# Kernel tuning notes

Hardware: AMD Instinct MI355X
Metric: run time of the kernel (lower is better)

## Reference

```python
import jax, jax.numpy as jnp
import numpy as np

B, S, D = 4, 1024, 1024
H = 16           # heads
HD = D // H      # head dim
E = 8            # experts
TOPK = 2
F = 4 * D        # expert ffn hidden


def setup_inputs() -> dict:
    key = jax.random.key(0)
    ks = jax.random.split(key, 8)
    w = lambda k, shp: jax.random.normal(k, shp, dtype=jnp.float32) * 0.02
    return {
        "x": jax.random.normal(ks[0], (B, S, D), dtype=jnp.float32),
        "ln1_g": jnp.ones((D,), jnp.float32), "ln1_b": jnp.zeros((D,), jnp.float32),
        "Wqkv": w(ks[1], (D, 3 * D)),
        "Wo": w(ks[2], (D, D)),
        "ln2_g": jnp.ones((D,), jnp.float32), "ln2_b": jnp.zeros((D,), jnp.float32),
        "Wg": w(ks[3], (D, E)),
        "W1": w(ks[4], (E, D, F)),
        "W2": w(ks[5], (E, F, D)),
    }


def _layernorm(x, g, b, eps=1e-5):
    mu = jnp.mean(x, axis=-1, keepdims=True)
    var = jnp.var(x, axis=-1, keepdims=True)
    return (x - mu) * jax.lax.rsqrt(var + eps) * g + b


def _attn(h, Wqkv, Wo):
    qkv = h @ Wqkv                                   # [B,S,3D]
    q, k, v = jnp.split(qkv, 3, axis=-1)
    q = q.reshape(B, S, H, HD)
    k = k.reshape(B, S, H, HD)
    v = v.reshape(B, S, H, HD)
    scores = jnp.einsum("bqhd,bkhd->bhqk", q, k) / np.sqrt(HD)
    causal = jnp.tril(jnp.ones((S, S), bool))
    scores = jnp.where(causal, scores, jnp.finfo(scores.dtype).min)
    p = jax.nn.softmax(scores, axis=-1)
    o = jnp.einsum("bhqk,bkhd->bqhd", p, v).reshape(B, S, D)
    return o @ Wo


def _moe(h, Wg, W1, W2):
    # h: [N, D] tokens; top-k softmax gating, dense all-expert reference
    logits = h @ Wg                                   # [N, E]
    top_vals, top_idx = jax.lax.top_k(logits, TOPK)   # [N, k]
    wts = jax.nn.softmax(top_vals, axis=-1)           # gate weights over top-k
    gates = jnp.sum(jax.nn.one_hot(top_idx, E) * wts[..., None], axis=1)  # [N, E]
    act = jax.nn.gelu(jnp.einsum("nd,edf->enf", h, W1))  # [E, N, F]
    eo = jnp.einsum("enf,efd->end", act, W2)             # [E, N, D]
    return jnp.einsum("ne,end->nd", gates, eo)           # combine


def reference(x, ln1_g, ln1_b, Wqkv, Wo, ln2_g, ln2_b, Wg, W1, W2):
    h = _layernorm(x, ln1_g, ln1_b)
    x_resid = x + _attn(h, Wqkv, Wo)
    moe_in = _layernorm(x_resid, ln2_g, ln2_b).reshape(B * S, D)
    y = _moe(moe_in, Wg, W1, W2).reshape(B, S, D)
    return x_resid + y
```

## Files before the change

kernel.cpp:

```cpp
#include <hip/hip_runtime.h>

typedef unsigned short u16;
typedef _Float16 f16x8 __attribute__((ext_vector_type(8)));
typedef __bf16   bf16x8 __attribute__((ext_vector_type(8)));
typedef float    f32x4 __attribute__((ext_vector_type(4)));

struct __align__(8) U16x4 { u16 v[4]; };

#define MAXT 72

__device__ __forceinline__ u16 f2b(float f) {
  unsigned u = __builtin_bit_cast(unsigned, f);
  return (u16)((u + 0x7FFFu + ((u >> 16) & 1u)) >> 16);
}
__device__ __forceinline__ u16 f2h(float f) { return __builtin_bit_cast(u16, (_Float16)f); }
__device__ __forceinline__ u16 f2h_lo(float f) {
  _Float16 h = (_Float16)f;
  return __builtin_bit_cast(u16, (_Float16)(f - (float)h));
}
__device__ __forceinline__ void llds16(const void* g, void* l) {
  __builtin_amdgcn_global_load_lds((const __attribute__((address_space(1))) unsigned int*)g,
                                   (__attribute__((address_space(3))) unsigned int*)l, 16, 0, 0);
}
__device__ __forceinline__ f32x4 mmf(f16x8 a, f16x8 b, f32x4 c) {
  return __builtin_amdgcn_mfma_f32_16x16x32_f16(a, b, c, 0, 0, 0);
}
__device__ __forceinline__ f32x4 mmb(bf16x8 a, bf16x8 b, f32x4 c) {
  return __builtin_amdgcn_mfma_f32_16x16x32_bf16(a, b, c, 0, 0, 0);
}

template<int OUT>
__global__ __launch_bounds__(256) void transpose_kernel(const float* __restrict__ src,
                                                        u16* __restrict__ d0, u16* __restrict__ d1,
                                                        int R, int C) {
  __shared__ float t[32][33];
  long zo = (long)blockIdx.z * R * C;
  int r0 = blockIdx.y << 5, c0 = blockIdx.x << 5;
  int tid = threadIdx.x;
  {
    int r = tid >> 3, c = (tid & 7) << 2;
    float4 v = *(const float4*)(src + zo + (long)(r0 + r) * C + c0 + c);
    t[r][c] = v.x; t[r][c + 1] = v.y; t[r][c + 2] = v.z; t[r][c + 3] = v.w;
  }
  __syncthreads();
  int c = tid >> 3, rg = (tid & 7) << 2;
  long o = zo + (long)(c0 + c) * R + r0 + rg;
  U16x4 a, b2;
#pragma unroll
  for (int i = 0; i < 4; i++) {
    float f = t[rg + i][c];
    if (OUT == 0) { a.v[i] = f2h(f); b2.v[i] = f2h_lo(f); }
    else a.v[i] = f2b(f);
  }
  *(U16x4*)(d0 + o) = a;
  if (OUT == 0) *(U16x4*)(d1 + o) = b2;
}

__global__ __launch_bounds__(256) void wg_transpose(const float* __restrict__ Wg,
                                                    float* __restrict__ WgT) {
  int idx = blockIdx.x * 256 + threadIdx.x;
  int d = idx >> 3, e = idx & 7;
  WgT[e * 1024 + d] = Wg[idx];
}

__global__ __launch_bounds__(256) void ln_kernel(const float* __restrict__ x, const float* __restrict__ g,
                                                 const float* __restrict__ bt,
                                                 u16* __restrict__ d0, u16* __restrict__ d1) {
  long row = blockIdx.x;
  int tid = threadIdx.x;
  const float4 v = *(const float4*)(x + (row << 10) + (tid << 2));
  float s = v.x + v.y + v.z + v.w;
  float q = v.x * v.x + v.y * v.y + v.z * v.z + v.w * v.w;
#pragma unroll
  for (int m = 1; m < 64; m <<= 1) { s += __shfl_xor(s, m); q += __shfl_xor(q, m); }
  __shared__ float rs[4], rq[4];
  if ((tid & 63) == 0) { rs[tid >> 6] = s; rq[tid >> 6] = q; }
  __syncthreads();
  s = rs[0] + rs[1] + rs[2] + rs[3];
  q = rq[0] + rq[1] + rq[2] + rq[3];
  float mu = s * (1.f / 1024.f);
  float inv = 1.f / sqrtf(q * (1.f / 1024.f) - mu * mu + 1e-5f);
  float4 gg = *(const float4*)(g + (tid << 2));
  float4 bb = *(const float4*)(bt + (tid << 2));
  float o0 = (v.x - mu) * inv * gg.x + bb.x;
  float o1 = (v.y - mu) * inv * gg.y + bb.y;
  float o2 = (v.z - mu) * inv * gg.z + bb.z;
  float o3 = (v.w - mu) * inv * gg.w + bb.w;
  long o = (row << 10) + (tid << 2);
  U16x4 a, b2;
  a.v[0] = f2h(o0); a.v[1] = f2h(o1); a.v[2] = f2h(o2); a.v[3] = f2h(o3);
  b2.v[0] = f2h_lo(o0); b2.v[1] = f2h_lo(o1); b2.v[2] = f2h_lo(o2); b2.v[3] = f2h_lo(o3);
  *(U16x4*)(d0 + o) = a; *(U16x4*)(d1 + o) = b2;
}

template<int MODE>
__global__ __launch_bounds__(512, 1) void gemm_kernel(
    const u16* __restrict__ Ah, const u16* __restrict__ Al,
    const u16* __restrict__ Bh, const u16* __restrict__ Bl,
    int K, int ldc, int Nexp,
    const int* __restrict__ lists, const int* __restrict__ tile_e,
    const int* __restrict__ tile_b, const int* __restrict__ tile_c,
    float* __restrict__ outf, u16* __restrict__ outb,
    const float* __restrict__ resid, const float* __restrict__ slotw) {
  constexpr bool SPLIT = (MODE < 2);
  constexpr int NP = SPLIT ? 4 : 2;
  constexpr int TN = (MODE == 1) ? 64 : 128;
  constexpr int NF = TN >> 6;
  constexpr int NB = TN >> 6;
  __shared__ u16 lds[NP][8192];
  const int tid = threadIdx.x, w = tid >> 6, l = tid & 63;
  int n0;
  int grbase = 0, rowsv = 128;
  long m0 = 0;
  if (MODE >= 2) {
    int lin = blockIdx.x;
    int c = lin & 7, k = lin >> 3;
    int ty = c * 9 + (k % 9);
    int tx = k / 9;
    n0 = tx * TN;
    int e = tile_e[ty];
    if (e < 0) return;
    grbase = tile_b[ty];
    rowsv = tile_c[ty];
    Bh += (long)e * Nexp * K;
  } else {
    n0 = blockIdx.x * TN;
    m0 = (long)blockIdx.y << 7;
  }

  const u16 *as0[2], *as1[2], *bs0[2], *bs1[2];
  int dstA[2], dstB[2];
#pragma unroll
  for (int i = 0; i < 2; i++) {
    int chunk = i * 512 + tid;
    int row = chunk >> 3, c16 = chunk & 7;
    int scol = (c16 << 4) ^ ((row & 7) << 4);
    dstA[i] = chunk << 4;
    long ar;
    if (MODE == 2) {
      int vlu = lists[(row < rowsv) ? (grbase + row) : grbase];
      ar = (long)(vlu >> 1);
    } else if (MODE == 3) {
      ar = grbase + ((row < rowsv) ? row : 0);
    } else {
      ar = m0 + row;
    }
    long ao = ar * (long)K + (scol >> 1);
    as0[i] = Ah + ao;
    if (SPLIT) as1[i] = Al + ao;
  }
#pragma unroll
  for (int i = 0; i < NB; i++) {
    int chunk = i * 512 + tid;
    int row = chunk >> 3, c16 = chunk & 7;
    int scol = (c16 << 4) ^ ((row & 7) << 4);
    dstB[i] = chunk << 4;
    long bo = (long)(n0 + row) * K + (scol >> 1);
    bs0[i] = Bh + bo;
    if (SPLIT) bs1[i] = Bl + bo;
  }

  f32x4 acc[4][NF];
#pragma unroll
  for (int i = 0; i < 4; i++)
#pragma unroll
    for (int j = 0; j < NF; j++) acc[i][j] = (f32x4){0.f, 0.f, 0.f, 0.f};

  const int wr = (w >> 2) << 6;
  const int wc = (w & 3) * (TN / 4);
  const int nkt = K >> 6;
  for (int kt = 0; kt < nkt; ++kt) {
    if (kt) __syncthreads();
#pragma unroll
    for (int i = 0; i < 2; i++) {
      llds16(as0[i] + (kt << 6), (char*)(&lds[0][0]) + dstA[i]);
      if (SPLIT) llds16(as1[i] + (kt << 6), (char*)(&lds[NP - 2][0]) + dstA[i]);
    }
#pragma unroll
    for (int i = 0; i < NB; i++) {
      llds16(bs0[i] + (kt << 6), (char*)(&lds[1][0]) + dstB[i]);
      if (SPLIT) llds16(bs1[i] + (kt << 6), (char*)(&lds[NP - 1][0]) + dstB[i]);
    }
    __syncthreads();
#pragma unroll
    for (int kc = 0; kc < 2; kc++) {
      const int kby = (kc << 6) + ((l >> 4) << 4);
      int aoff[4], boff[NF];
#pragma unroll
      for (int mf = 0; mf < 4; mf++) { int row = wr + (mf << 4) + (l & 15); aoff[mf] = (row << 7) + (kby ^ ((row & 7) << 4)); }
#pragma unroll
      for (int nf = 0; nf < NF; nf++) { int row = wc + (nf << 4) + (l & 15); boff[nf] = (row << 7) + (kby ^ ((row & 7) << 4)); }
      if (SPLIT) {
        f16x8 a0[4], a1[4], b0[NF], b1[NF];
#pragma unroll
        for (int mf = 0; mf < 4; mf++) {
          a0[mf] = *(const f16x8*)((const char*)(&lds[0][0]) + aoff[mf]);
          a1[mf] = *(const f16x8*)((const char*)(&lds[NP - 2][0]) + aoff[mf]);
        }
#pragma unroll
        for (int nf = 0; nf < NF; nf++) {
          b0[nf] = *(const f16x8*)((const char*)(&lds[1][0]) + boff[nf]);
          b1[nf] = *(const f16x8*)((const char*)(&lds[NP - 1][0]) + boff[nf]);
        }
#pragma unroll
        for (int mf = 0; mf < 4; mf++)
#pragma unroll
          for (int nf = 0; nf < NF; nf++) {
            acc[mf][nf] = mmf(a0[mf], b0[nf], acc[mf][nf]);
            acc[mf][nf] = mmf(a0[mf], b1[nf], acc[mf][nf]);
            acc[mf][nf] = mmf(a1[mf], b0[nf], acc[mf][nf]);
          }
      } else {
        bf16x8 a0[4], b0[NF];
#pragma unroll
        for (int mf = 0; mf < 4; mf++) a0[mf] = *(const bf16x8*)((const char*)(&lds[0][0]) + aoff[mf]);
#pragma unroll
        for (int nf = 0; nf < NF; nf++) b0[nf] = *(const bf16x8*)((const char*)(&lds[1][0]) + boff[nf]);
#pragma unroll
        for (int mf = 0; mf < 4; mf++)
#pragma unroll
          for (int nf = 0; nf < NF; nf++) acc[mf][nf] = mmb(a0[mf], b0[nf], acc[mf][nf]);
      }
    }
  }

#pragma unroll
  for (int mf = 0; mf < 4; mf++) {
#pragma unroll
    for (int r = 0; r < 4; r++) {
      const int lrow = wr + (mf << 4) + ((l >> 4) << 2) + r;
      if (MODE >= 2 && lrow >= rowsv) continue;
      float gw = 0.f; long orow = 0;
      if (MODE == 3) { int gr = grbase + lrow; orow = (long)lists[gr] * ldc; gw = slotw[gr]; }
#pragma unroll
      for (int nf = 0; nf < NF; nf++) {
        const int col = n0 + wc + (nf << 4) + (l & 15);
        float v = acc[mf][nf][r];
        if (MODE == 0) {
          outf[(m0 + lrow) * (long)ldc + col] = v;
        } else if (MODE == 1) {
          long ix = (m0 + lrow) * (long)ldc + col;
          outf[ix] = v + resid[ix];
        } else if (MODE == 2) {
          float t = v * (1.59576912f + 0.07135539f * v * v);
          float u = v * __builtin_amdgcn_rcpf(1.f + __expf(-t));
          outb[(long)(grbase + lrow) * ldc + col] = f2b(u);
        } else {
          outf[orow + col] = v * gw;
        }
      }
    }
  }
}

__global__ __launch_bounds__(256) void kv_prep(const float* __restrict__ qkv,
                                               u16* __restrict__ Kh, u16* __restrict__ Kl,
                                               u16* __restrict__ Vth, u16* __restrict__ Vtl) {
  __shared__ float t[64][65];
  const int tid = threadIdx.x;
  const int kb = blockIdx.x, h = blockIdx.y, b = blockIdx.z;
  const long bb = ((long)b) << 10;
  const int hoff = h << 6;
  const long head = ((long)(b * 16 + h)) << 16;
  {
    int rr = tid >> 4, c = (tid & 15) << 2;
#pragma unroll
    for (int p = 0; p < 4; p++) {
      int r = rr + p * 16;
      const float* base = qkv + (bb + kb * 64 + r) * 3072 + hoff + c;
      float4 u = *(const float4*)(base + 1024);
      U16x4 a, lo;
      a.v[0] = f2h(u.x); a.v[1] = f2h(u.y); a.v[2] = f2h(u.z); a.v[3] = f2h(u.w);
      lo.v[0] = f2h_lo(u.x); lo.v[1] = f2h_lo(u.y); lo.v[2] = f2h_lo(u.z); lo.v[3] = f2h_lo(u.w);
      long o = head + (long)(kb * 64 + r) * 64 + c;
      *(U16x4*)(Kh + o) = a; *(U16x4*)(Kl + o) = lo;
      float4 v = *(const float4*)(base + 2048);
      t[r][c] = v.x; t[r][c + 1] = v.y; t[r][c + 2] = v.z; t[r][c + 3] = v.w;
    }
  }
  __syncthreads();
  {
    int hd = tid >> 2, k4 = (tid & 3) << 4;
#pragma unroll
    for (int q = 0; q < 4; q++) {
      U16x4 a, lo;
#pragma unroll
      for (int j = 0; j < 4; j++) {
        float f = t[k4 + q * 4 + j][hd];
        a.v[j] = f2h(f); lo.v[j] = f2h_lo(f);
      }
      long o = head + (long)hd * 1024 + kb * 64 + k4 + q * 4;
      *(U16x4*)(Vth + o) = a; *(U16x4*)(Vtl + o) = lo;
    }
  }
}

__global__ __launch_bounds__(256, 1) void attn_kernel(const float* __restrict__ qkv,
                                                      const u16* __restrict__ Kh, const u16* __restrict__ Kl,
                                                      const u16* __restrict__ Vth, const u16* __restrict__ Vtl,
                                                      u16* __restrict__ oh, u16* __restrict__ ol) {
  __shared__ u16 kh[4096], kl[4096];
  __shared__ u16 vh[4096], vl[4096];
  __shared__ u16 ph[4][1024], pl[4][1024];
  const int tid = threadIdx.x, w = tid >> 6, l = tid & 63;
  const int qbi = blockIdx.x, hh_ = blockIdx.y, b = blockIdx.z;
  const long bb = ((long)b) << 10;
  const int hoff = hh_ << 6;
  const long head = ((long)(b * 16 + hh_)) << 16;

  const u16 *ks0[2], *ks1[2], *vs0[2], *vs1[2];
  int db[2];
#pragma unroll
  for (int i = 0; i < 2; i++) {
    int chunk = i * 256 + tid;
    int row = chunk >> 3, c16 = chunk & 7;
    int sc = ((c16 << 4) ^ ((row & 7) << 4)) >> 1;
    db[i] = chunk << 4;
    ks0[i] = Kh + head + row * 64 + sc;
    ks1[i] = Kl + head + row * 64 + sc;
    vs0[i] = Vth + head + (long)row * 1024 + sc;
    vs1[i] = Vtl + head + (long)row * 1024 + sc;
  }

  for (int pass = 0; pass < 2; ++pass) {
    const int qb = (pass ? qbi : (15 - qbi)) << 6;
    f16x8 q0[2], q1[2];
    {
      const long qrow = bb + qb + (w << 4) + (l & 15);
      const float* qp = qkv + qrow * 3072 + hoff + ((l >> 4) << 3);
#pragma unroll
      for (int kc = 0; kc < 2; kc++) {
        float4 u0 = *(const float4*)(qp + (kc << 5));
        float4 u1 = *(const float4*)(qp + (kc << 5) + 4);
        float vv[8] = {u0.x, u0.y, u0.z, u0.w, u1.x, u1.y, u1.z, u1.w};
#pragma unroll
        for (int j = 0; j < 8; j++) {
          _Float16 hi = (_Float16)vv[j];
          q0[kc][j] = hi;
          q1[kc][j] = (_Float16)(vv[j] - (float)hi);
        }
      }
    }

    f32x4 o[4];
#pragma unroll
    for (int nf = 0; nf < 4; nf++) o[nf] = (f32x4){0.f, 0.f, 0.f, 0.f};
    float mr[4] = {-1e30f, -1e30f, -1e30f, -1e30f};
    float lr[4] = {0.f, 0.f, 0.f, 0.f};
    const int ktm = qb >> 6;

    for (int kt = 0; kt <= ktm; ++kt) {
      __syncthreads();
#pragma unroll
      for (int i = 0; i < 2; i++) {
        llds16(ks0[i] + (kt << 12), (char*)kh + db[i]);
        llds16(ks1[i] + (kt << 12), (char*)kl + db[i]);
        llds16(vs0[i] + (kt << 6), (char*)vh + db[i]);
        llds16(vs1[i] + (kt << 6), (char*)vl + db[i]);
      }
      __syncthreads();

      f32x4 s[4];
#pragma unroll
      for (int nf = 0; nf < 4; nf++) s[nf] = (f32x4){0.f, 0.f, 0.f, 0.f};
#pragma unroll
      for (int kc = 0; kc < 2; kc++) {
        const int kby = (kc << 6) + ((l >> 4) << 4);
#pragma unroll
        for (int nf = 0; nf < 4; nf++) {
          int row = (nf << 4) + (l & 15);
          int off = (row << 7) + (kby ^ ((row & 7) << 4));
          f16x8 k0 = *(const f16x8*)((const char*)kh + off);
          f16x8 k1 = *(const f16x8*)((const char*)kl + off);
          s[nf] = mmf(q0[kc], k0, s[nf]);
          s[nf] = mmf(q0[kc], k1, s[nf]);
          s[nf] = mmf(q1[kc], k0, s[nf]);
        }
      }
      const bool lastt = (kt == ktm);
#pragma unroll
      for (int nf = 0; nf < 4; nf++)
#pragma unroll
        for (int r = 0; r < 4; r++) {
          float sc = s[nf][r] * 0.125f;
          if (lastt) {
            int keyg = (kt << 6) + (nf << 4) + (l & 15);
            int qg = qb + (w << 4) + ((l >> 4) << 2) + r;
            if (keyg > qg) sc = -1e30f;
          }
          s[nf][r] = sc;
        }
      float alpha[4];
#pragma unroll
      for (int r = 0; r < 4; r++) {
        float mx = fmaxf(fmaxf(s[0][r], s[1][r]), fmaxf(s[2][r], s[3][r]));
        mx = fmaxf(mx, __shfl_xor(mx, 1));
        mx = fmaxf(mx, __shfl_xor(mx, 2));
        mx = fmaxf(mx, __shfl_xor(mx, 4));
        mx = fmaxf(mx, __shfl_xor(mx, 8));
        float mn = fmaxf(mr[r], mx);
        float su = 0.f;
#pragma unroll
        for (int nf = 0; nf < 4; nf++) { float pv = __expf(s[nf][r] - mn); s[nf][r] = pv; su += pv; }
        su += __shfl_xor(su, 1); su += __shfl_xor(su, 2);
        su += __shfl_xor(su, 4); su += __shfl_xor(su, 8);
        alpha[r] = __expf(mr[r] - mn);
        lr[r] = lr[r] * alpha[r] + su;
        mr[r] = mn;
      }
#pragma unroll
      for (int nf = 0; nf < 4; nf++)
#pragma unroll
        for (int r = 0; r < 4; r++) o[nf][r] *= alpha[r];
#pragma unroll
      for (int nf = 0; nf < 4; nf++)
#pragma unroll
        for (int r = 0; r < 4; r++) {
          int m = ((l >> 4) << 2) + r, k = (nf << 4) + (l & 15);
          int off = (m << 7) + ((k << 1) ^ ((m & 7) << 4));
          float pv = s[nf][r];
          _Float16 hi = (_Float16)pv;
          *(u16*)((char*)&ph[w][0] + off) = __builtin_bit_cast(u16, hi);
          *(u16*)((char*)&pl[w][0] + off) = __builtin_bit_cast(u16, (_Float16)(pv - (float)hi));
        }
#pragma unroll
      for (int kc = 0; kc < 2; kc++) {
        const int kby = (kc << 6) + ((l >> 4) << 4);
        const int mm = l & 15;
        int poff = (mm << 7) + (kby ^ ((mm & 7) << 4));
        f16x8 p0 = *(const f16x8*)((const char*)&ph[w][0] + poff);
        f16x8 p1 = *(const f16x8*)((const char*)&pl[w][0] + poff);
#pragma unroll
        for (int nf = 0; nf < 4; nf++) {
          int row = (nf << 4) + (l & 15);
          int off = (row << 7) + (kby ^ ((row & 7) << 4));
          f16x8 v0 = *(const f16x8*)((const char*)vh + off);
          f16x8 v1 = *(const f16x8*)((const char*)vl + off);
          o[nf] = mmf(p0, v0, o[nf]);
          o[nf] = mmf(p0, v1, o[nf]);
          o[nf] = mmf(p1, v0, o[nf]);
        }
      }
    }
#pragma unroll
    for (int nf = 0; nf < 4; nf++)
#pragma unroll
      for (int r = 0; r < 4; r++) {
        int lrow = (w << 4) + ((l >> 4) << 2) + r;
        float v = o[nf][r] / lr[r];
        long ix = (bb + qb + lrow) * 1024 + hoff + (nf << 4) + (l & 15);
        _Float16 hi = (_Float16)v;
        oh[ix] = __builtin_bit_cast(u16, hi);
        ol[ix] = __builtin_bit_cast(u16, (_Float16)(v - (float)hi));
      }
  }
}

__global__ __launch_bounds__(256) void gate_kernel(const float* __restrict__ xr, const float* __restrict__ g,
                                                   const float* __restrict__ b, const float* __restrict__ WgT,
                                                   int* __restrict__ tok_e, float* __restrict__ tok_w,
                                                   u16* __restrict__ moe) {
  int w = threadIdx.x >> 6, l = threadIdx.x & 63;
  long t = (long)blockIdx.x * 4 + w;
  const float* row = xr + (t << 10);
  float4 xv[4]; float s = 0.f, q = 0.f;
#pragma unroll
  for (int i = 0; i < 4; i++) {
    float4 v = *(const float4*)(row + (i << 8) + (l << 2));
    xv[i] = v;
    s += v.x + v.y + v.z + v.w;
    q += v.x * v.x + v.y * v.y + v.z * v.z + v.w * v.w;
  }
#pragma unroll
  for (int m = 1; m < 64; m <<= 1) { s += __shfl_xor(s, m); q += __shfl_xor(q, m); }
  float mu = s * (1.f / 1024.f);
  float inv = 1.f / sqrtf(q * (1.f / 1024.f) - mu * mu + 1e-5f);
  float acc[8] = {0.f, 0.f, 0.f, 0.f, 0.f, 0.f, 0.f, 0.f};
#pragma unroll
  for (int i = 0; i < 4; i++) {
    int d0 = (i << 8) + (l << 2);
    float4 gg = *(const float4*)(g + d0);
    float4 bb = *(const float4*)(b + d0);
    float x0 = (xv[i].x - mu) * inv * gg.x + bb.x;
    float x1 = (xv[i].y - mu) * inv * gg.y + bb.y;
    float x2 = (xv[i].z - mu) * inv * gg.z + bb.z;
    float x3 = (xv[i].w - mu) * inv * gg.w + bb.w;
    U16x4 st;
    st.v[0] = f2b(x0); st.v[1] = f2b(x1); st.v[2] = f2b(x2); st.v[3] = f2b(x3);
    *(U16x4*)(moe + (t << 10) + d0) = st;
#pragma unroll
    for (int e = 0; e < 8; e++) {
      float4 wq = *(const float4*)(WgT + (e << 10) + d0);
      acc[e] += x0 * wq.x + x1 * wq.y + x2 * wq.z + x3 * wq.w;
    }
  }
#pragma unroll
  for (int e = 0; e < 8; e++)
#pragma unroll
    for (int m = 1; m < 64; m <<= 1) acc[e] += __shfl_xor(acc[e], m);
  if (l == 0) {
    int e0 = 0; float v0 = acc[0];
#pragma unroll
    for (int e = 1; e < 8; e++) if (acc[e] > v0) { v0 = acc[e]; e0 = e; }
    int e1 = (e0 == 0) ? 1 : 0; float v1 = acc[e1];
#pragma unroll
    for (int e = 0; e < 8; e++) if (e != e0 && acc[e] > v1) { v1 = acc[e]; e1 = e; }
    float w0 = 1.f / (1.f + __expf(v1 - v0));
    tok_e[t * 2] = e0; tok_e[t * 2 + 1] = e1;
    tok_w[t * 2] = w0; tok_w[t * 2 + 1] = 1.f - w0;
  }
}

__global__ __launch_bounds__(256) void plan_kernel(const int* __restrict__ tok_e, int* __restrict__ cursor,
                                                   int* __restrict__ tile_e, int* __restrict__ tile_b,
                                                   int* __restrict__ tile_c) {
  __shared__ int wc[4][8];
  int tid = threadIdx.x, w = tid >> 6, l = tid & 63;
  int c0 = 0, c1 = 0, c2 = 0, c3 = 0, c4 = 0, c5 = 0, c6 = 0, c7 = 0;
  for (int k = 0; k < 32; k++) {
    int v = tok_e[(w << 11) + (k << 6) + l];
    c0 += (v == 0); c1 += (v == 1); c2 += (v == 2); c3 += (v == 3);
    c4 += (v == 4); c5 += (v == 5); c6 += (v == 6); c7 += (v == 7);
  }
#pragma unroll
  for (int m = 1; m < 64; m <<= 1) {
    c0 += __shfl_xor(c0, m); c1 += __shfl_xor(c1, m); c2 += __shfl_xor(c2, m); c3 += __shfl_xor(c3, m);
    c4 += __shfl_xor(c4, m); c5 += __shfl_xor(c5, m); c6 += __shfl_xor(c6, m); c7 += __shfl_xor(c7, m);
  }
  if (l == 0) {
    wc[w][0] = c0; wc[w][1] = c1; wc[w][2] = c2; wc[w][3] = c3;
    wc[w][4] = c4; wc[w][5] = c5; wc[w][6] = c6; wc[w][7] = c7;
  }
  __syncthreads();
  if (tid == 0) {
    int o = 0, t2 = 0;
    for (int e = 0; e < 8; e++) {
      cursor[e] = o;
      int cc = wc[0][e] + wc[1][e] + wc[2][e] + wc[3][e];
      for (int i = 0; i < cc; i += 128) {
        tile_e[t2] = e; tile_b[t2] = o + i; tile_c[t2] = (cc - i < 128) ? (cc - i) : 128; t2++;
      }
      o += cc;
    }
    for (; t2 < MAXT; t2++) tile_e[t2] = -1;
  }
}

__global__ __launch_bounds__(256) void scatter_kernel(const int* __restrict__ tok_e, const float* __restrict__ tok_w,
                                                      int* __restrict__ cursor, int* __restrict__ lists,
                                                      float* __restrict__ slotw) {
  int t = blockIdx.x * 256 + threadIdx.x;
#pragma unroll
  for (int s = 0; s < 2; s++) {
    int e = tok_e[t * 2 + s];
    int pos = atomicAdd(&cursor[e], 1);
    lists[pos] = t * 2 + s;
    slotw[pos] = tok_w[t * 2 + s];
  }
}

__global__ __launch_bounds__(256) void combine_kernel(float* __restrict__ out, const float* __restrict__ yp) {
  long i = (long)blockIdx.x * 256 + threadIdx.x;
  long n = i >> 8;
  long d = i & 255;
  float4 o = *(float4*)(out + (i << 2));
  const float4 a = *(const float4*)(yp + ((n * 2) << 10) + (d << 2));
  const float4 b = *(const float4*)(yp + ((n * 2 + 1) << 10) + (d << 2));
  o.x += a.x + b.x; o.y += a.y + b.y; o.z += a.z + b.z; o.w += a.w + b.w;
  *(float4*)(out + (i << 2)) = o;
}

extern "C" void kernel_launch(void* const* d_in, const int* in_sizes, int n_in,
                              void* d_out, int out_size, void* d_ws, size_t ws_size,
                              hipStream_t stream) {
  const float* x    = (const float*)d_in[0];
  const float* ln1g = (const float*)d_in[1];
  const float* ln1b = (const float*)d_in[2];
  const float* Wqkv = (const float*)d_in[3];
  const float* Wo   = (const float*)d_in[4];
  const float* ln2g = (const float*)d_in[5];
  const float* ln2b = (const float*)d_in[6];
  const float* Wg   = (const float*)d_in[7];
  const float* W1   = (const float*)d_in[8];
  const float* W2   = (const float*)d_in[9];
  float* out = (float*)d_out;
  char* ws = (char*)d_ws;

  size_t off = 0;
  auto alloc = [&](size_t b) { size_t o = off; off += (b + 255) & ~size_t(255); return o; };
  u16* WqkvTh = (u16*)(ws + alloc(3072ull * 1024 * 2));
  u16* WqkvTl = (u16*)(ws + alloc(3072ull * 1024 * 2));
  u16* WoTh   = (u16*)(ws + alloc(1024ull * 1024 * 2));
  u16* WoTl   = (u16*)(ws + alloc(1024ull * 1024 * 2));
  u16* W1T    = (u16*)(ws + alloc(8ull * 4096 * 1024 * 2));
  u16* W2T    = (u16*)(ws + alloc(8ull * 1024 * 4096 * 2));
  u16* hh     = (u16*)(ws + alloc(4096ull * 1024 * 2));
  u16* hl     = (u16*)(ws + alloc(4096ull * 1024 * 2));
  float* qkv  = (float*)(ws + alloc(4096ull * 3072 * 4));
  u16* atth   = (u16*)(ws + alloc(4096ull * 1024 * 2));
  u16* attl   = (u16*)(ws + alloc(4096ull * 1024 * 2));
  u16* moein  = (u16*)(ws + alloc(4096ull * 1024 * 2));
  u16* act    = (u16*)(ws + alloc(8192ull * 4096 * 2));
  float* WgT  = (float*)(ws + alloc(8ull * 1024 * 4));
  float* ypart = qkv;
  u16* Kh  = act;
  u16* Kl  = act + 4194304;
  u16* Vth = act + 2 * 4194304;
  u16* Vtl = act + 3 * 4194304;
  int* tok_e  = (int*)(ws + alloc(8192 * 4));
  float* tok_w = (float*)(ws + alloc(8192 * 4));
  int* cursor = (int*)(ws + alloc(64));
  int* lists  = (int*)(ws + alloc(8192 * 4));
  float* slotw = (float*)(ws + alloc(8192 * 4));
  int* tile_e = (int*)(ws + alloc(MAXT * 4));
  int* tile_b = (int*)(ws + alloc(MAXT * 4));
  int* tile_c = (int*)(ws + alloc(MAXT * 4));
  (void)in_sizes; (void)n_in; (void)out_size; (void)ws_size;

  dim3 blk(256), blk512(512);
  transpose_kernel<0><<<dim3(96, 32, 1), blk, 0, stream>>>(Wqkv, WqkvTh, WqkvTl, 1024, 3072);
  transpose_kernel<0><<<dim3(32, 32, 1), blk, 0, stream>>>(Wo, WoTh, WoTl, 1024, 1024);
  transpose_kernel<1><<<dim3(128, 32, 8), blk, 0, stream>>>(W1, W1T, nullptr, 1024, 4096);
  transpose_kernel<1><<<dim3(32, 128, 8), blk, 0, stream>>>(W2, W2T, nullptr, 4096, 1024);
  wg_transpose<<<dim3(32), blk, 0, stream>>>(Wg, WgT);
  ln_kernel<<<dim3(4096), blk, 0, stream>>>(x, ln1g, ln1b, hh, hl);
  gemm_kernel<0><<<dim3(24, 32), blk512, 0, stream>>>(hh, hl, WqkvTh, WqkvTl, 1024, 3072, 0,
                                                      nullptr, nullptr, nullptr, nullptr,
                                                      qkv, nullptr, nullptr, nullptr);
  kv_prep<<<dim3(16, 16, 4), blk, 0, stream>>>(qkv, Kh, Kl, Vth, Vtl);
  attn_kernel<<<dim3(8, 16, 4), blk, 0, stream>>>(qkv, Kh, Kl, Vth, Vtl, atth, attl);
  gemm_kernel<1><<<dim3(16, 32), blk512, 0, stream>>>(atth, attl, WoTh, WoTl, 1024, 1024, 0,
                                                      nullptr, nullptr, nullptr, nullptr,
                                                      out, nullptr, x, nullptr);
  gate_kernel<<<dim3(1024), blk, 0, stream>>>(out, ln2g, ln2b, WgT, tok_e, tok_w, moein);
  plan_kernel<<<dim3(1), blk, 0, stream>>>(tok_e, cursor, tile_e, tile_b, tile_c);
  scatter_kernel<<<dim3(16), blk, 0, stream>>>(tok_e, tok_w, cursor, lists, slotw);
  gemm_kernel<2><<<dim3(8 * 9 * 32), blk512, 0, stream>>>(moein, nullptr, W1T, nullptr, 1024, 4096, 4096,
                                                          lists, tile_e, tile_b, tile_c,
                                                          nullptr, act, nullptr, nullptr);
  gemm_kernel<3><<<dim3(8 * 9 * 8), blk512, 0, stream>>>(act, nullptr, W2T, nullptr, 4096, 1024, 1024,
                                                         lists, tile_e, tile_b, tile_c,
                                                         ypart, nullptr, nullptr, slotw);
  combine_kernel<<<dim3(4096), blk, 0, stream>>>(out, ypart);
}
```

Before: 541.4 us.

## Double-buffer LDS tiles in bf16 expert GEMM to overlap loads with MFMA

For the non-split bf16 GEMM modes (the MoE expert matmuls), the K loop now uses two LDS buffers. It prefetches tile kt+1 with global_load_lds while computing on tile kt, which cuts one barrier per iteration and hides global load latency. The split fp16 path is unchanged but now always allocates a 4-buffer LDS array. The cost is more LDS per block, which is fine at one block per CU. It relies on the barrier at the end of each iteration to order the async LDS writes against reads.

```diff
diff --git a/kernel.cpp b/kernel.cpp
--- a/kernel.cpp
+++ b/kernel.cpp
@@ -103,11 +103,10 @@
     float* __restrict__ outf, u16* __restrict__ outb,
     const float* __restrict__ resid, const float* __restrict__ slotw) {
   constexpr bool SPLIT = (MODE < 2);
-  constexpr int NP = SPLIT ? 4 : 2;
   constexpr int TN = (MODE == 1) ? 64 : 128;
   constexpr int NF = TN >> 6;
   constexpr int NB = TN >> 6;
-  __shared__ u16 lds[NP][8192];
+  __shared__ u16 lds[4][8192];
   const int tid = threadIdx.x, w = tid >> 6, l = tid & 63;
   int n0;
   int grbase = 0, rowsv = 128;
@@ -169,38 +168,39 @@
   const int wr = (w >> 2) << 6;
   const int wc = (w & 3) * (TN / 4);
   const int nkt = K >> 6;
-  for (int kt = 0; kt < nkt; ++kt) {
-    if (kt) __syncthreads();
-#pragma unroll
-    for (int i = 0; i < 2; i++) {
-      llds16(as0[i] + (kt << 6), (char*)(&lds[0][0]) + dstA[i]);
-      if (SPLIT) llds16(as1[i] + (kt << 6), (char*)(&lds[NP - 2][0]) + dstA[i]);
-    }
-#pragma unroll
-    for (int i = 0; i < NB; i++) {
-      llds16(bs0[i] + (kt << 6), (char*)(&lds[1][0]) + dstB[i]);
-      if (SPLIT) llds16(bs1[i] + (kt << 6), (char*)(&lds[NP - 1][0]) + dstB[i]);
-    }
-    __syncthreads();
-#pragma unroll
-    for (int kc = 0; kc < 2; kc++) {
-      const int kby = (kc << 6) + ((l >> 4) << 4);
-      int aoff[4], boff[NF];
-#pragma unroll
-      for (int mf = 0; mf < 4; mf++) { int row = wr + (mf << 4) + (l & 15); aoff[mf] = (row << 7) + (kby ^ ((row & 7) << 4)); }
-#pragma unroll
-      for (int nf = 0; nf < NF; nf++) { int row = wc + (nf << 4) + (l & 15); boff[nf] = (row << 7) + (kby ^ ((row & 7) << 4)); }
-      if (SPLIT) {
+
+  if constexpr (SPLIT) {
+    for (int kt = 0; kt < nkt; ++kt) {
+      if (kt) __syncthreads();
+#pragma unroll
+      for (int i = 0; i < 2; i++) {
+        llds16(as0[i] + (kt << 6), (char*)(&lds[0][0]) + dstA[i]);
+        llds16(as1[i] + (kt << 6), (char*)(&lds[2][0]) + dstA[i]);
+      }
+#pragma unroll
+      for (int i = 0; i < NB; i++) {
+        llds16(bs0[i] + (kt << 6), (char*)(&lds[1][0]) + dstB[i]);
+        llds16(bs1[i] + (kt << 6), (char*)(&lds[3][0]) + dstB[i]);
+      }
+      __syncthreads();
+#pragma unroll
+      for (int kc = 0; kc < 2; kc++) {
+        const int kby = (kc << 6) + ((l >> 4) << 4);
+        int aoff[4], boff[NF];
+#pragma unroll
+        for (int mf = 0; mf < 4; mf++) { int row = wr + (mf << 4) + (l & 15); aoff[mf] = (row << 7) + (kby ^ ((row & 7) << 4)); }
+#pragma unroll
+        for (int nf = 0; nf < NF; nf++) { int row = wc + (nf << 4) + (l & 15); boff[nf] = (row << 7) + (kby ^ ((row & 7) << 4)); }
         f16x8 a0[4], a1[4], b0[NF], b1[NF];
 #pragma unroll
         for (int mf = 0; mf < 4; mf++) {
           a0[mf] = *(const f16x8*)((const char*)(&lds[0][0]) + aoff[mf]);
-          a1[mf] = *(const f16x8*)((const char*)(&lds[NP - 2][0]) + aoff[mf]);
+          a1[mf] = *(const f16x8*)((const char*)(&lds[2][0]) + aoff[mf]);
         }
 #pragma unroll
         for (int nf = 0; nf < NF; nf++) {
           b0[nf] = *(const f16x8*)((const char*)(&lds[1][0]) + boff[nf]);
-          b1[nf] = *(const f16x8*)((const char*)(&lds[NP - 1][0]) + boff[nf]);
+          b1[nf] = *(const f16x8*)((const char*)(&lds[3][0]) + boff[nf]);
         }
 #pragma unroll
         for (int mf = 0; mf < 4; mf++)
@@ -210,17 +210,46 @@
             acc[mf][nf] = mmf(a0[mf], b1[nf], acc[mf][nf]);
             acc[mf][nf] = mmf(a1[mf], b0[nf], acc[mf][nf]);
           }
-      } else {
+      }
+    }
+  } else {
+#pragma unroll
+    for (int i = 0; i < 2; i++) llds16(as0[i], (char*)(&lds[0][0]) + dstA[i]);
+#pragma unroll
+    for (int i = 0; i < NB; i++) llds16(bs0[i], (char*)(&lds[1][0]) + dstB[i]);
+    __syncthreads();
+    int cur = 0;
+    for (int kt = 0; kt < nkt; ++kt) {
+      if (kt + 1 < nkt) {
+        const int nb = (cur ^ 1) << 1;
+#pragma unroll
+        for (int i = 0; i < 2; i++) llds16(as0[i] + ((kt + 1) << 6), (char*)(&lds[nb][0]) + dstA[i]);
+#pragma unroll
+        for (int i = 0; i < NB; i++) llds16(bs0[i] + ((kt + 1) << 6), (char*)(&lds[nb + 1][0]) + dstB[i]);
+      }
+      const char* pA = (const char*)(&lds[cur << 1][0]);
+      const char* pB = (const char*)(&lds[(cur << 1) + 1][0]);
+#pragma unroll
+      for (int kc = 0; kc < 2; kc++) {
+        const int kby = (kc << 6) + ((l >> 4) << 4);
         bf16x8 a0[4], b0[NF];
 #pragma unroll
-        for (int mf = 0; mf < 4; mf++) a0[mf] = *(const bf16x8*)((const char*)(&lds[0][0]) + aoff[mf]);
-#pragma unroll
-        for (int nf = 0; nf < NF; nf++) b0[nf] = *(const bf16x8*)((const char*)(&lds[1][0]) + boff[nf]);
+        for (int mf = 0; mf < 4; mf++) {
+          int row = wr + (mf << 4) + (l & 15);
+          a0[mf] = *(const bf16x8*)(pA + (row << 7) + (kby ^ ((row & 7) << 4)));
+        }
+#pragma unroll
+        for (int nf = 0; nf < NF; nf++) {
+          int row = wc + (nf << 4) + (l & 15);
+          b0[nf] = *(const bf16x8*)(pB + (row << 7) + (kby ^ ((row & 7) << 4)));
+        }
 #pragma unroll
         for (int mf = 0; mf < 4; mf++)
 #pragma unroll
           for (int nf = 0; nf < NF; nf++) acc[mf][nf] = mmb(a0[mf], b0[nf], acc[mf][nf]);
       }
+      __syncthreads();
+      cur ^= 1;
     }
   }
 
```

After: 568.3 us. 1.05x slower.

## Use 64-row expert tiles for the MoE down-projection GEMM

Applied to the files above, without the earlier changes.

The expert down-projection GEMM (MODE 3) now uses 64-row M tiles with one 16-column fragment per wave, instead of 128-row tiles. A second tile plan with up to 136 entries is built in plan_kernel, and the launch grid grows to match. LDS is sized per mode. The aim is to cut wasted rows in partially filled expert tiles and raise block count for better CU load balance. In exchange, W2 is streamed twice as often and each wave issues fewer MFMAs per LDS load.

```diff
diff --git a/kernel.cpp b/kernel.cpp
--- a/kernel.cpp
+++ b/kernel.cpp
@@ -8,6 +8,7 @@
 struct __align__(8) U16x4 { u16 v[4]; };
 
 #define MAXT 72
+#define MAXT2 136
 
 __device__ __forceinline__ u16 f2b(float f) {
   unsigned u = __builtin_bit_cast(unsigned, f);
@@ -103,20 +104,28 @@
     float* __restrict__ outf, u16* __restrict__ outb,
     const float* __restrict__ resid, const float* __restrict__ slotw) {
   constexpr bool SPLIT = (MODE < 2);
-  constexpr int NP = SPLIT ? 4 : 2;
   constexpr int TN = (MODE == 1) ? 64 : 128;
-  constexpr int NF = TN >> 6;
+  constexpr int BM = (MODE == 3) ? 64 : 128;
+  constexpr int NF = (MODE == 3) ? 1 : (TN >> 6);
+  constexpr int NA = BM >> 6;
   constexpr int NB = TN >> 6;
-  __shared__ u16 lds[NP][8192];
+  constexpr int ABYT = SPLIT ? 16384 : BM * 128;
+  constexpr int SMEM = SPLIT ? 65536 : (BM + TN) * 128;
+  __shared__ __align__(16) char smem[SMEM];
+  char* pAh = smem;
+  char* pBh = smem + ABYT;
+  char* pAl = smem + 32768;
+  char* pBl = smem + 49152;
   const int tid = threadIdx.x, w = tid >> 6, l = tid & 63;
   int n0;
-  int grbase = 0, rowsv = 128;
+  int grbase = 0, rowsv = BM;
   long m0 = 0;
   if (MODE >= 2) {
+    constexpr int TPX = (MODE == 3) ? 17 : 9;
     int lin = blockIdx.x;
     int c = lin & 7, k = lin >> 3;
-    int ty = c * 9 + (k % 9);
-    int tx = k / 9;
+    int ty = c * TPX + (k % TPX);
+    int tx = k / TPX;
     n0 = tx * TN;
     int e = tile_e[ty];
     if (e < 0) return;
@@ -131,7 +140,7 @@
   const u16 *as0[2], *as1[2], *bs0[2], *bs1[2];
   int dstA[2], dstB[2];
 #pragma unroll
-  for (int i = 0; i < 2; i++) {
+  for (int i = 0; i < NA; i++) {
     int chunk = i * 512 + tid;
     int row = chunk >> 3, c16 = chunk & 7;
     int scol = (c16 << 4) ^ ((row & 7) << 4);
@@ -166,20 +175,21 @@
 #pragma unroll
     for (int j = 0; j < NF; j++) acc[i][j] = (f32x4){0.f, 0.f, 0.f, 0.f};
 
-  const int wr = (w >> 2) << 6;
-  const int wc = (w & 3) * (TN / 4);
+  int wr, wc;
+  if (MODE == 3) { wr = 0; wc = w << 4; }
+  else { wr = (w >> 2) << 6; wc = (w & 3) * (TN / 4); }
   const int nkt = K >> 6;
   for (int kt = 0; kt < nkt; ++kt) {
     if (kt) __syncthreads();
 #pragma unroll
-    for (int i = 0; i < 2; i++) {
-      llds16(as0[i] + (kt << 6), (char*)(&lds[0][0]) + dstA[i]);
-      if (SPLIT) llds16(as1[i] + (kt << 6), (char*)(&lds[NP - 2][0]) + dstA[i]);
+    for (int i = 0; i < NA; i++) {
+      llds16(as0[i] + (kt << 6), pAh + dstA[i]);
+      if (SPLIT) llds16(as1[i] + (kt << 6), pAl + dstA[i]);
     }
 #pragma unroll
     for (int i = 0; i < NB; i++) {
-      llds16(bs0[i] + (kt << 6), (char*)(&lds[1][0]) + dstB[i]);
-      if (SPLIT) llds16(bs1[i] + (kt << 6), (char*)(&lds[NP - 1][0]) + dstB[i]);
+      llds16(bs0[i] + (kt << 6), pBh + dstB[i]);
+      if (SPLIT) llds16(bs1[i] + (kt << 6), pBl + dstB[i]);
     }
     __syncthreads();
 #pragma unroll
@@ -194,13 +204,13 @@
         f16x8 a0[4], a1[4], b0[NF], b1[NF];
 #pragma unroll
         for (int mf = 0; mf < 4; mf++) {
-          a0[mf] = *(const f16x8*)((const char*)(&lds[0][0]) + aoff[mf]);
-          a1[mf] = *(const f16x8*)((const char*)(&lds[NP - 2][0]) + aoff[mf]);
+          a0[mf] = *(const f16x8*)(pAh + aoff[mf]);
+          a1[mf] = *(const f16x8*)(pAl + aoff[mf]);
         }
 #pragma unroll
         for (int nf = 0; nf < NF; nf++) {
-          b0[nf] = *(const f16x8*)((const char*)(&lds[1][0]) + boff[nf]);
-          b1[nf] = *(const f16x8*)((const char*)(&lds[NP - 1][0]) + boff[nf]);
+          b0[nf] = *(const f16x8*)(pBh + boff[nf]);
+          b1[nf] = *(const f16x8*)(pBl + boff[nf]);
         }
 #pragma unroll
         for (int mf = 0; mf < 4; mf++)
@@ -213,9 +223,9 @@
       } else {
         bf16x8 a0[4], b0[NF];
 #pragma unroll
-        for (int mf = 0; mf < 4; mf++) a0[mf] = *(const bf16x8*)((const char*)(&lds[0][0]) + aoff[mf]);
-#pragma unroll
-        for (int nf = 0; nf < NF; nf++) b0[nf] = *(const bf16x8*)((const char*)(&lds[1][0]) + boff[nf]);
+        for (int mf = 0; mf < 4; mf++) a0[mf] = *(const bf16x8*)(pAh + aoff[mf]);
+#pragma unroll
+        for (int nf = 0; nf < NF; nf++) b0[nf] = *(const bf16x8*)(pBh + boff[nf]);
 #pragma unroll
         for (int mf = 0; mf < 4; mf++)
 #pragma unroll
@@ -513,7 +523,9 @@
 
 __global__ __launch_bounds__(256) void plan_kernel(const int* __restrict__ tok_e, int* __restrict__ cursor,
                                                    int* __restrict__ tile_e, int* __restrict__ tile_b,
-                                                   int* __restrict__ tile_c) {
+                                                   int* __restrict__ tile_c,
+                                                   int* __restrict__ tile2_e, int* __restrict__ tile2_b,
+                                                   int* __restrict__ tile2_c) {
   __shared__ int wc[4][8];
   int tid = threadIdx.x, w = tid >> 6, l = tid & 63;
   int c0 = 0, c1 = 0, c2 = 0, c3 = 0, c4 = 0, c5 = 0, c6 = 0, c7 = 0;
@@ -533,16 +545,20 @@
   }
   __syncthreads();
   if (tid == 0) {
-    int o = 0, t2 = 0;
+    int o = 0, t1 = 0, t2 = 0;
     for (int e = 0; e < 8; e++) {
       cursor[e] = o;
       int cc = wc[0][e] + wc[1][e] + wc[2][e] + wc[3][e];
       for (int i = 0; i < cc; i += 128) {
-        tile_e[t2] = e; tile_b[t2] = o + i; tile_c[t2] = (cc - i < 128) ? (cc - i) : 128; t2++;
+        tile_e[t1] = e; tile_b[t1] = o + i; tile_c[t1] = (cc - i < 128) ? (cc - i) : 128; t1++;
+      }
+      for (int i = 0; i < cc; i += 64) {
+        tile2_e[t2] = e; tile2_b[t2] = o + i; tile2_c[t2] = (cc - i < 64) ? (cc - i) : 64; t2++;
       }
       o += cc;
     }
-    for (; t2 < MAXT; t2++) tile_e[t2] = -1;
+    for (; t1 < MAXT; t1++) tile_e[t1] = -1;
+    for (; t2 < MAXT2; t2++) tile2_e[t2] = -1;
   }
 }
 
@@ -615,6 +631,9 @@
   int* tile_e = (int*)(ws + alloc(MAXT * 4));
   int* tile_b = (int*)(ws + alloc(MAXT * 4));
   int* tile_c = (int*)(ws + alloc(MAXT * 4));
+  int* tile2_e = (int*)(ws + alloc(MAXT2 * 4));
+  int* tile2_b = (int*)(ws + alloc(MAXT2 * 4));
+  int* tile2_c = (int*)(ws + alloc(MAXT2 * 4));
   (void)in_sizes; (void)n_in; (void)out_size; (void)ws_size;
 
   dim3 blk(256), blk512(512);
@@ -633,13 +652,14 @@
                                                       nullptr, nullptr, nullptr, nullptr,
                                                       out, nullptr, x, nullptr);
   gate_kernel<<<dim3(1024), blk, 0, stream>>>(out, ln2g, ln2b, WgT, tok_e, tok_w, moein);
-  plan_kernel<<<dim3(1), blk, 0, stream>>>(tok_e, cursor, tile_e, tile_b, tile_c);
+  plan_kernel<<<dim3(1), blk, 0, stream>>>(tok_e, cursor, tile_e, tile_b, tile_c,
+                                           tile2_e, tile2_b, tile2_c);
   scatter_kernel<<<dim3(16), blk, 0, stream>>>(tok_e, tok_w, cursor, lists, slotw);
   gemm_kernel<2><<<dim3(8 * 9 * 32), blk512, 0, stream>>>(moein, nullptr, W1T, nullptr, 1024, 4096, 4096,
                                                           lists, tile_e, tile_b, tile_c,
                                                           nullptr, act, nullptr, nullptr);
-  gemm_kernel<3><<<dim3(8 * 9 * 8), blk512, 0, stream>>>(act, nullptr, W2T, nullptr, 4096, 1024, 1024,
-                                                         lists, tile_e, tile_b, tile_c,
-                                                         ypart, nullptr, nullptr, slotw);
+  gemm_kernel<3><<<dim3(8 * 17 * 8), blk512, 0, stream>>>(act, nullptr, W2T, nullptr, 4096, 1024, 1024,
+                                                          lists, tile2_e, tile2_b, tile2_c,
+                                                          ypart, nullptr, nullptr, slotw);
   combine_kernel<<<dim3(4096), blk, 0, stream>>>(out, ypart);
 }
```

After: 580.1 us. 7.1% more time.
